# Optimization experiments

Hardware: AMD Instinct MI355X
Metric: run time of the kernel (lower is better)

The kernel has to match this reference:

```python
import jax, jax.numpy as jnp
import numpy as np

EPS = 1e-5
K = 20  # n. neighbors


def _lrelu(x):
    return jnp.where(x >= 0, x, 0.2 * x)


def _bn(x, gamma, beta):
    # training-mode batchnorm over all axes except channel axis 1
    axes = tuple(i for i in range(x.ndim) if i != 1)
    m = jnp.mean(x, axis=axes, keepdims=True)
    v = jnp.var(x, axis=axes, keepdims=True)
    shape = [1, x.shape[1]] + [1] * (x.ndim - 2)
    return (x - m) * jax.lax.rsqrt(v + EPS) * gamma.reshape(shape) + beta.reshape(shape)


def _knn(x, k):
    # x: (B, C, N) -> idx (B, N, k) of nearest neighbors (largest negative sq dist)
    xx = jnp.sum(x * x, axis=1)                      # (B, N)
    inner = jnp.einsum('bcn,bcm->bnm', x, x)          # (B, N, N)
    dist = -xx[:, :, None] + 2.0 * inner - xx[:, None, :]
    _, idx = jax.lax.top_k(dist, k)
    return idx


def _graph_feature(x, k):
    # x: (B, C, N) -> edge features (B, 2C, N, k)
    B = x.shape[0]
    idx = _knn(x, k)                                  # (B, N, k)
    xt = jnp.transpose(x, (0, 2, 1))                  # (B, N, C)
    nbr = xt[jnp.arange(B)[:, None, None], idx]       # (B, N, k, C)
    ctr = xt[:, :, None, :]                           # (B, N, 1, C)
    edge = jnp.concatenate([nbr - ctr, jnp.broadcast_to(ctr, nbr.shape)], axis=-1)
    return jnp.transpose(edge, (0, 3, 1, 2))          # (B, 2C, N, k)


def _conv1d(W, x):
    return jnp.einsum('oc,bcn->bon', W, x)


def _conv2d(W, x):
    return jnp.einsum('oc,bcnk->bonk', W, x)


def setup_inputs() -> dict:
    key = jax.random.key(0)
    ks = jax.random.split(key, 10)
    w = lambda k, s: jax.random.normal(k, s, jnp.float32) * 0.05
    d = {
        'x': jax.random.normal(ks[0], (4, 3, 4096), jnp.float32),
        'W1': w(ks[1], (64, 3)),
        'W2': w(ks[2], (64, 128)),
        'W3': w(ks[3], (64, 128)),
        'W4': w(ks[4], (512, 64)),
        'W5': w(ks[5], (512, 704)),
        'W6': w(ks[6], (256, 512)),
        'W7': w(ks[7], (128, 256)),
        'W8': w(ks[8], (2, 128)),
        'bias8': jnp.zeros((2,), jnp.float32),
    }
    bn_ch = [64, 64, 64, 512, 512, 256, 128]
    for i, c in enumerate(bn_ch, start=1):
        d[f'gamma{i}'] = jnp.ones((c,), jnp.float32)
        d[f'beta{i}'] = jnp.zeros((c,), jnp.float32)
    return d


def reference(x, W1, W2, W3, W4, W5, W6, W7, W8, bias8,
              gamma1, beta1, gamma2, beta2, gamma3, beta3, gamma4, beta4,
              gamma5, beta5, gamma6, beta6, gamma7, beta7):
    N = x.shape[2]
    x1 = _lrelu(_bn(_conv1d(W1, x), gamma1, beta1))                 # (B,64,N)
    e2 = _graph_feature(x1, K)                                      # (B,128,N,k)
    x2 = _lrelu(_bn(_conv2d(W2, e2), gamma2, beta2)).max(axis=-1)   # (B,64,N)
    e3 = _graph_feature(x2, K)
    x3 = _lrelu(_bn(_conv2d(W3, e3), gamma3, beta3)).max(axis=-1)   # (B,64,N)
    x6 = _lrelu(_bn(_conv1d(W4, x3), gamma4, beta4))                # (B,512,N)
    x6 = jnp.broadcast_to(x6.max(axis=-1, keepdims=True), (x6.shape[0], x6.shape[1], N))
    x7 = jnp.concatenate([x1, x2, x3, x6], axis=1)                  # (B,704,N)
    x7 = _lrelu(_bn(_conv1d(W5, x7), gamma5, beta5))
    x7 = _lrelu(_bn(_conv1d(W6, x7), gamma6, beta6))
    x7 = _lrelu(_bn(_conv1d(W7, x7), gamma7, beta7))
    return _conv1d(W8, x7) + bias8[None, :, None]                   # (B,2,N)
```

## Files before the change

### kernel.cpp

```cpp
#include <hip/hip_runtime.h>
#include <math.h>

#define NN 4096
#define BB 4
#define NPT (NN*BB)
#define KK 20
#define EPSB 1e-5f

#define AS_STRIDE 132
#define WS_STRIDE 68
#define SKEW(c) ((((((c)>>2)&7))<<2) + (((c)>>5)*28))

__device__ __forceinline__ float lrelu(float x){ return x >= 0.f ? x : 0.2f*x; }

__device__ __forceinline__ unsigned fkey(float x){
  unsigned u = __float_as_uint(x);
  return u ^ (unsigned)(((int)u >> 31) | 0x80000000);
}

__global__ void conv1_kernel(const float* __restrict__ x, const float* __restrict__ W1,
                             float* __restrict__ xcat){
  __shared__ float Wl[192];
  int tid = threadIdx.x;
  if (tid < 192) Wl[tid] = W1[tid];
  __syncthreads();
  int p = blockIdx.x*4 + (tid >> 6);
  int o = tid & 63;
  int b = p >> 12, n = p & 4095;
  const float* xb = x + (size_t)b*3*NN + n;
  float acc = Wl[o*3+0]*xb[0] + Wl[o*3+1]*xb[NN] + Wl[o*3+2]*xb[2*NN];
  xcat[(size_t)p*192 + o] = acc;
}

__global__ void stats_pm_kernel(const float* __restrict__ buf, int stride, int ofs,
                                float* __restrict__ psum, float* __restrict__ psumsq, int C){
  int tid = threadIdx.x;
  int lane = tid & 63, g = tid >> 6;
  int o = blockIdx.x*64 + lane;
  int p0 = blockIdx.y*256 + g*64;
  float s = 0.f, ss = 0.f;
  for (int i = 0; i < 64; ++i){
    float v = buf[(size_t)(p0+i)*stride + ofs + o];
    s += v; ss += v*v;
  }
  __shared__ float rs[4][64], rss[4][64];
  rs[g][lane] = s; rss[g][lane] = ss;
  __syncthreads();
  if (g == 0){
    s  = rs[0][lane]+rs[1][lane]+rs[2][lane]+rs[3][lane];
    ss = rss[0][lane]+rss[1][lane]+rss[2][lane]+rss[3][lane];
    psum[(size_t)blockIdx.y*C + o] = s;
    psumsq[(size_t)blockIdx.y*C + o] = ss;
  }
}

__global__ void bn_finalize_kernel(const float* __restrict__ psum, const float* __restrict__ psumsq,
                                   int nparts,
                                   const float* __restrict__ gamma, const float* __restrict__ beta,
                                   float* __restrict__ scale, float* __restrict__ shift,
                                   float invcnt, int C){
  int o = threadIdx.x + blockIdx.x*blockDim.x;
  if (o >= C) return;
  float s = 0.f, ss = 0.f;
  for (int i = 0; i < nparts; ++i){
    s  += psum[(size_t)i*C + o];
    ss += psumsq[(size_t)i*C + o];
  }
  float m = s*invcnt;
  float v = ss*invcnt - m*m;
  v = fmaxf(v, 0.f);
  float sc = gamma[o] * rsqrtf(v + EPSB);
  scale[o] = sc;
  shift[o] = beta[o] - m*sc;
}

__global__ void apply_bn_kernel(float* __restrict__ buf, int stride, int ofs, int log2C,
                                const float* __restrict__ scale, const float* __restrict__ shift){
  int i = blockIdx.x*256 + threadIdx.x;
  int o = i & ((1<<log2C)-1);
  int p = i >> log2C;
  size_t a = (size_t)p*stride + ofs + o;
  float e = buf[a]*scale[o] + shift[o];
  buf[a] = lrelu(e);
}

__global__ void xx_kernel(const float* __restrict__ xcat, int stride, int ofs,
                          float* __restrict__ xx){
  int p = blockIdx.x*256 + threadIdx.x;
  const float4* r = (const float4*)(xcat + (size_t)p*stride + ofs);
  float s = 0.f;
  #pragma unroll
  for (int i = 0; i < 16; ++i){ float4 v = r[i]; s += v.x*v.x + v.y*v.y + v.z*v.z + v.w*v.w; }
  xx[p] = s;
}

__global__ void __launch_bounds__(256, 2)
dist_kernel(const float* __restrict__ xcat, int ofs,
            const float* __restrict__ xx, float* __restrict__ dist,
            unsigned* __restrict__ gmaxp, int b){
  int bx = blockIdx.x, by = blockIdx.y;
  if (by > bx) return;
  __shared__ float As[64*AS_STRIDE + 64];
  __shared__ float Bs[64*AS_STRIDE + 64];
  int tid = threadIdx.x;
  int n0 = by*128, m0 = bx*128;
  const float* base = xcat + (size_t)b*NN*192 + ofs;
  int cgrp = (tid & 15)*4;
  float4 vin[8], vw[8];
  #pragma unroll
  for (int j = 0; j < 8; ++j){
    int row = (tid + 256*j) >> 4;
    vin[j] = *(const float4*)(base + (size_t)(n0+row)*192 + cgrp);
    vw[j]  = *(const float4*)(base + (size_t)(m0+row)*192 + cgrp);
  }
  #pragma unroll
  for (int j = 0; j < 8; ++j){
    int row = (tid + 256*j) >> 4, c4 = cgrp;
    float4 v = vin[j];
    As[(c4+0)*AS_STRIDE+SKEW(c4+0)+row]=v.x; As[(c4+1)*AS_STRIDE+SKEW(c4+1)+row]=v.y;
    As[(c4+2)*AS_STRIDE+SKEW(c4+2)+row]=v.z; As[(c4+3)*AS_STRIDE+SKEW(c4+3)+row]=v.w;
    float4 w = vw[j];
    Bs[(c4+0)*AS_STRIDE+SKEW(c4+0)+row]=w.x; Bs[(c4+1)*AS_STRIDE+SKEW(c4+1)+row]=w.y;
    Bs[(c4+2)*AS_STRIDE+SKEW(c4+2)+row]=w.z; Bs[(c4+3)*AS_STRIDE+SKEW(c4+3)+row]=w.w;
  }
  __syncthreads();
  int pA = (tid >> 4)*4, oB = (tid & 15)*4;
  float acc[8][8] = {};
  for (int c = 0; c < 64; ++c){
    const float* arow = &As[c*AS_STRIDE + SKEW(c)];
    const float* brow = &Bs[c*AS_STRIDE + SKEW(c)];
    float4 a0 = *(const float4*)&arow[pA];
    float4 a1 = *(const float4*)&arow[pA + 64];
    float4 b0 = *(const float4*)&brow[oB];
    float4 b1 = *(const float4*)&brow[oB + 64];
    float av[8] = {a0.x,a0.y,a0.z,a0.w,a1.x,a1.y,a1.z,a1.w};
    float bv[8] = {b0.x,b0.y,b0.z,b0.w,b1.x,b1.y,b1.z,b1.w};
    #pragma unroll
    for (int i = 0; i < 8; ++i)
      #pragma unroll
      for (int j = 0; j < 8; ++j)
        acc[i][j] += av[i]*bv[j];
  }
  float xmv[8], xnv[8];
  #pragma unroll
  for (int j = 0; j < 4; ++j){
    xmv[j]   = xx[b*NN + m0 + oB + j];
    xmv[4+j] = xx[b*NN + m0 + 64 + oB + j];
    xnv[j]   = xx[b*NN + n0 + pA + j];
    xnv[4+j] = xx[b*NN + n0 + 64 + pA + j];
  }
  #pragma unroll
  for (int h = 0; h < 2; ++h){
    #pragma unroll
    for (int i = 0; i < 4; ++i){
      int row = n0 + h*64 + pA + i;
      float xn = xnv[h*4 + i];
      int ai = h*4 + i;
      float4 w0, w1;
      w0.x = 2.f*acc[ai][0] - xn - xmv[0]; w0.y = 2.f*acc[ai][1] - xn - xmv[1];
      w0.z = 2.f*acc[ai][2] - xn - xmv[2]; w0.w = 2.f*acc[ai][3] - xn - xmv[3];
      w1.x = 2.f*acc[ai][4] - xn - xmv[4]; w1.y = 2.f*acc[ai][5] - xn - xmv[5];
      w1.z = 2.f*acc[ai][6] - xn - xmv[6]; w1.w = 2.f*acc[ai][7] - xn - xmv[7];
      float* drow = dist + (size_t)row*NN + m0;
      *(float4*)(drow + oB) = w0;
      *(float4*)(drow + 64 + oB) = w1;
      unsigned gm = fkey(w0.x), t;
      t = fkey(w0.y); if (t > gm) gm = t;
      t = fkey(w0.z); if (t > gm) gm = t;
      t = fkey(w0.w); if (t > gm) gm = t;
      t = fkey(w1.x); if (t > gm) gm = t;
      t = fkey(w1.y); if (t > gm) gm = t;
      t = fkey(w1.z); if (t > gm) gm = t;
      t = fkey(w1.w); if (t > gm) gm = t;
      gmaxp[(size_t)row*512 + (bx<<4) + (oB>>2)] = gm;
    }
  }
  if (bx != by){
    #pragma unroll
    for (int jh = 0; jh < 2; ++jh){
      #pragma unroll
      for (int jj = 0; jj < 4; ++jj){
        int j = jh*4 + jj;
        float xm = xmv[j];
        float4 lo, hi;
        lo.x = 2.f*acc[0][j] - xm - xnv[0];
        lo.y = 2.f*acc[1][j] - xm - xnv[1];
        lo.z = 2.f*acc[2][j] - xm - xnv[2];
        lo.w = 2.f*acc[3][j] - xm - xnv[3];
        hi.x = 2.f*acc[4][j] - xm - xnv[4];
        hi.y = 2.f*acc[5][j] - xm - xnv[5];
        hi.z = 2.f*acc[6][j] - xm - xnv[6];
        hi.w = 2.f*acc[7][j] - xm - xnv[7];
        int mrow = m0 + jh*64 + oB + jj;
        float* drow = dist + (size_t)mrow*NN + n0;
        *(float4*)(drow + pA) = lo;
        *(float4*)(drow + 64 + pA) = hi;
        unsigned gm = fkey(lo.x), t;
        t = fkey(lo.y); if (t > gm) gm = t;
        t = fkey(lo.z); if (t > gm) gm = t;
        t = fkey(lo.w); if (t > gm) gm = t;
        t = fkey(hi.x); if (t > gm) gm = t;
        t = fkey(hi.y); if (t > gm) gm = t;
        t = fkey(hi.z); if (t > gm) gm = t;
        t = fkey(hi.w); if (t > gm) gm = t;
        gmaxp[(size_t)mrow*512 + (by<<4) + (pA>>2)] = gm;
      }
    }
  }
}

__global__ void __launch_bounds__(256)
topk_kernel(const float* __restrict__ dist, const unsigned* __restrict__ gmax,
            int* __restrict__ idxout){
  __shared__ unsigned lv[4][256], li[4][256];
  __shared__ unsigned lcnt[4];
  int wv = threadIdx.x >> 6, lane = threadIdx.x & 63;
  int n = blockIdx.x*4 + wv;
  const unsigned* grow = gmax + (size_t)n*512;
  unsigned g[8];
  #pragma unroll
  for (int j = 0; j < 8; ++j) g[j] = grow[j*64 + lane];
  if (lane == 0) lcnt[wv] = 0u;
  unsigned prefix = 0u, act = 0xFFu; int need = KK; int tot = 512;
  for (int b = 31; b >= 16; --b){
    unsigned m = 0u;
    #pragma unroll
    for (int j = 0; j < 8; ++j) m |= ((g[j] >> b) & 1u) << j;
    unsigned c = (unsigned)__popc(m & act);
    #pragma unroll
    for (int s = 1; s < 64; s <<= 1) c += __shfl_xor(c, s);
    if ((int)c >= need){ act &= m; prefix |= (1u << b); tot = (int)c; }
    else { need -= (int)c; act &= ~m; tot -= (int)c; }
    if (KK - need + tot <= 44) break;
  }
  unsigned T = prefix;
  const float* drow = dist + (size_t)n*NN;
  #pragma unroll
  for (int j = 0; j < 8; ++j){
    if (g[j] >= T){
      int gid = j*64 + lane;
      int cbase = ((gid >> 4) << 7) + ((gid & 15) << 2);
      float4 v0 = *(const float4*)(drow + cbase);
      float4 v1 = *(const float4*)(drow + cbase + 64);
      unsigned k0=fkey(v0.x),k1=fkey(v0.y),k2=fkey(v0.z),k3=fkey(v0.w);
      unsigned k4=fkey(v1.x),k5=fkey(v1.y),k6=fkey(v1.z),k7=fkey(v1.w);
      int q = (k0>=T)+(k1>=T)+(k2>=T)+(k3>=T)+(k4>=T)+(k5>=T)+(k6>=T)+(k7>=T);
      unsigned pos = atomicAdd(&lcnt[wv], (unsigned)q);
      #define PUTC(kx,cofs) if (kx >= T){ if (pos < 256u){ lv[wv][pos]=kx; li[wv][pos]=(unsigned)(cbase+(cofs)); } pos++; }
      PUTC(k0,0) PUTC(k1,1) PUTC(k2,2) PUTC(k3,3)
      PUTC(k4,64) PUTC(k5,65) PUTC(k6,66) PUTC(k7,67)
      #undef PUTC
    }
  }
  unsigned C = lcnt[wv];
  int* orow = idxout + (size_t)n*KK;
  if (C <= 64u){
    unsigned kv = 0u, ki = 0xFFFFFFFFu;
    if (lane < (int)C){ kv = lv[wv][lane]; ki = li[wv][lane]; }
    #pragma unroll
    for (int k = 2; k <= 64; k <<= 1){
      #pragma unroll
      for (int j2 = k >> 1; j2 > 0; j2 >>= 1){
        unsigned ov = __shfl_xor(kv, j2);
        unsigned oi = __shfl_xor(ki, j2);
        bool iLower = ((lane & j2) == 0);
        bool dirDesc = ((lane & k) == 0);
        bool mineGr = (kv > ov) || (kv == ov && ki < oi);
        bool keep = dirDesc ? (iLower ? mineGr : !mineGr)
                            : (iLower ? !mineGr : mineGr);
        kv = keep ? kv : ov;
        ki = keep ? ki : oi;
      }
    }
    if (lane < KK) orow[lane] = (int)ki;
  } else {
    unsigned rv[KK], ri[KK];
    #pragma unroll
    for (int q = 0; q < KK; ++q){ rv[q]=0u; ri[q]=0xFFFFFFFFu; }
    #pragma unroll
    for (int j = 0; j < 8; ++j){
      if (g[j] >= T){
        int gid = j*64 + lane;
        int cbase = ((gid >> 4) << 7) + ((gid & 15) << 2);
        float4 v0 = *(const float4*)(drow + cbase);
        float4 v1 = *(const float4*)(drow + cbase + 64);
        float f0[8] = {v0.x,v0.y,v0.z,v0.w,v1.x,v1.y,v1.z,v1.w};
        #pragma unroll
        for (int t = 0; t < 8; ++t){
          unsigned u = fkey(f0[t]);
          unsigned ix = (unsigned)(cbase + ((t < 4) ? t : (60 + t)));
          bool beat = (u > rv[KK-1]) || (u == rv[KK-1] && ix < ri[KK-1]);
          if (u >= T && beat){
            unsigned pv = u, pi = ix;
            #pragma unroll
            for (int p = 0; p < KK; ++p){
              bool keep2 = (rv[p] > pv) || (rv[p] == pv && ri[p] < pi);
              unsigned nv = keep2 ? rv[p] : pv;
              unsigned ni = keep2 ? ri[p] : pi;
              pv = keep2 ? pv : rv[p];
              pi = keep2 ? pi : ri[p];
              rv[p] = nv; ri[p] = ni;
            }
          }
        }
      }
    }
    for (int q = 0; q < KK; ++q){
      unsigned bv = rv[0], bi = ri[0];
      #pragma unroll
      for (int s = 1; s < 64; s <<= 1){
        unsigned ov = __shfl_xor(bv, s);
        unsigned oi = __shfl_xor(bi, s);
        bool take = (ov > bv) || (ov == bv && oi < bi);
        bv = take ? ov : bv;
        bi = take ? oi : bi;
      }
      if (rv[0] == bv && ri[0] == bi){
        #pragma unroll
        for (int p = 0; p < KK-1; ++p){ rv[p] = rv[p+1]; ri[p] = ri[p+1]; }
        rv[KK-1] = 0u; ri[KK-1] = 0xFFFFFFFFu;
      }
      if (lane == 0) orow[q] = (int)bi;
    }
  }
}

__global__ void ut_kernel(const float* __restrict__ xcat, int ofs, const float* __restrict__ W,
                          float* __restrict__ U, float* __restrict__ T){
  __shared__ float Wl[64*129];
  int tid = threadIdx.x;
  for (int i = tid; i < 64*128; i += 256){
    int o = i >> 7, c = i & 127;
    Wl[o*129 + c] = W[i];
  }
  __syncthreads();
  int g = tid >> 6, lane = tid & 63;
  int p = blockIdx.x*4 + g;
  float xv = xcat[(size_t)p*192 + ofs + lane];
  const float* wr = Wl + lane*129;
  float u = 0.f, t = 0.f;
  for (int c = 0; c < 64; ++c){
    float xc = __shfl(xv, c);
    float wa = wr[c], wb = wr[64+c];
    u += wa*xc;
    t += (wb - wa)*xc;
  }
  U[(size_t)p*64 + lane] = u;
  T[(size_t)p*64 + lane] = t;
}

__global__ void gather_kernel(const float* __restrict__ U, const float* __restrict__ T,
                              const int* __restrict__ idx,
                              float* __restrict__ psum, float* __restrict__ psumsq,
                              float* __restrict__ vmax, float* __restrict__ vmin){
  int tid = threadIdx.x;
  int g = tid >> 6, lane = tid & 63;
  int p0 = blockIdx.x*64 + g*16;
  float s = 0.f, ss = 0.f;
  for (int pi = 0; pi < 16; ++pi){
    int p = p0 + pi;
    int base = (p >> 12) << 12;
    float t = T[(size_t)p*64 + lane];
    const int* ir = idx + (size_t)p*KK;
    float mx = -INFINITY, mn = INFINITY;
    for (int k = 0; k < KK; ++k){
      int j = ir[k];
      float v = U[(size_t)(base + j)*64 + lane] + t;
      s += v; ss += v*v;
      mx = fmaxf(mx, v); mn = fminf(mn, v);
    }
    vmax[(size_t)p*64 + lane] = mx;
    vmin[(size_t)p*64 + lane] = mn;
  }
  __shared__ float rs[4][64], rss[4][64];
  rs[g][lane] = s; rss[g][lane] = ss;
  __syncthreads();
  if (g == 0){
    s  = rs[0][lane]+rs[1][lane]+rs[2][lane]+rs[3][lane];
    ss = rss[0][lane]+rss[1][lane]+rss[2][lane]+rss[3][lane];
    psum[(size_t)blockIdx.x*64 + lane] = s;
    psumsq[(size_t)blockIdx.x*64 + lane] = ss;
  }
}

__global__ void gapply_kernel(const float* __restrict__ vmax, const float* __restrict__ vmin,
                              const float* __restrict__ scale, const float* __restrict__ shift,
                              float* __restrict__ xcat, int ofs){
  int i = blockIdx.x*256 + threadIdx.x;
  int p = i >> 6, o = i & 63;
  float s = scale[o];
  float v = (s >= 0.f) ? vmax[i] : vmin[i];
  xcat[(size_t)p*192 + ofs + o] = lrelu(s*v + shift[o]);
}

__global__ void __launch_bounds__(256, 2)
mm_kernel(const float* __restrict__ in, int inStride, int inOfs,
          const float* __restrict__ W, int wStride,
          float* __restrict__ out, int outStride,
          const float* __restrict__ bias, int O, int I,
          const float* __restrict__ bnScale, const float* __restrict__ bnShift){
  __shared__ float As[64*AS_STRIDE + 64];
  __shared__ float Ws[64*WS_STRIDE + 64];
  int tid = threadIdx.x;
  int p0 = blockIdx.x*128, o0 = blockIdx.y*64;
  int psub = (tid >> 4)*8, osub = (tid & 15)*4;
  int cgrp = (tid & 15)*4;
  float acc[8][4] = {};
  for (int cc = 0; cc < I; cc += 64){
    float4 sc4 = make_float4(1.f,1.f,1.f,1.f), sh4 = make_float4(0.f,0.f,0.f,0.f);
    if (bnScale){
      sc4 = *(const float4*)(bnScale + cc + cgrp);
      sh4 = *(const float4*)(bnShift + cc + cgrp);
    }
    float4 vin[8], vw[4];
    #pragma unroll
    for (int j = 0; j < 8; ++j){
      int row = (tid + 256*j) >> 4;
      vin[j] = *(const float4*)(in + (size_t)(p0+row)*inStride + inOfs + cc + cgrp);
    }
    #pragma unroll
    for (int j = 0; j < 4; ++j){
      int row = (tid + 256*j) >> 4;
      vw[j] = *(const float4*)(W + (size_t)(o0+row)*wStride + cc + cgrp);
    }
    #pragma unroll
    for (int j = 0; j < 8; ++j){
      int row = (tid + 256*j) >> 4, c4 = cgrp;
      float4 v = vin[j];
      if (bnScale){
        v.x = lrelu(v.x*sc4.x + sh4.x); v.y = lrelu(v.y*sc4.y + sh4.y);
        v.z = lrelu(v.z*sc4.z + sh4.z); v.w = lrelu(v.w*sc4.w + sh4.w);
      }
      As[(c4+0)*AS_STRIDE+SKEW(c4+0)+row]=v.x; As[(c4+1)*AS_STRIDE+SKEW(c4+1)+row]=v.y;
      As[(c4+2)*AS_STRIDE+SKEW(c4+2)+row]=v.z; As[(c4+3)*AS_STRIDE+SKEW(c4+3)+row]=v.w;
    }
    #pragma unroll
    for (int j = 0; j < 4; ++j){
      int row = (tid + 256*j) >> 4, c4 = cgrp;
      float4 v = vw[j];
      Ws[(c4+0)*WS_STRIDE+SKEW(c4+0)+row]=v.x; Ws[(c4+1)*WS_STRIDE+SKEW(c4+1)+row]=v.y;
      Ws[(c4+2)*WS_STRIDE+SKEW(c4+2)+row]=v.z; Ws[(c4+3)*WS_STRIDE+SKEW(c4+3)+row]=v.w;
    }
    __syncthreads();
    for (int c = 0; c < 64; ++c){
      const float* arow = &As[c*AS_STRIDE + SKEW(c)];
      const float* brow = &Ws[c*WS_STRIDE + SKEW(c)];
      float4 a0 = *(const float4*)&arow[psub];
      float4 a1 = *(const float4*)&arow[psub + 4];
      float4 bb = *(const float4*)&brow[osub];
      float av[8] = {a0.x,a0.y,a0.z,a0.w,a1.x,a1.y,a1.z,a1.w};
      float bv[4] = {bb.x,bb.y,bb.z,bb.w};
      #pragma unroll
      for (int i = 0; i < 8; ++i)
        #pragma unroll
        for (int j = 0; j < 4; ++j)
          acc[i][j] += av[i]*bv[j];
    }
    __syncthreads();
  }
  int bIdx = p0 >> 12;
  float bb0=0.f, bb1=0.f, bb2=0.f, bb3=0.f;
  if (bias){
    bb0 = bias[bIdx*O + o0 + osub + 0];
    bb1 = bias[bIdx*O + o0 + osub + 1];
    bb2 = bias[bIdx*O + o0 + osub + 2];
    bb3 = bias[bIdx*O + o0 + osub + 3];
  }
  #pragma unroll
  for (int i = 0; i < 8; ++i){
    float4 w;
    w.x = acc[i][0]+bb0; w.y = acc[i][1]+bb1; w.z = acc[i][2]+bb2; w.w = acc[i][3]+bb3;
    *(float4*)(out + (size_t)(p0+psub+i)*outStride + o0 + osub) = w;
  }
}

__global__ void __launch_bounds__(256, 2)
mm128_kernel(const float* __restrict__ in, int inStride, int inOfs,
             const float* __restrict__ W, int wStride,
             float* __restrict__ out, int outStride,
             const float* __restrict__ bias, int O, int I,
             const float* __restrict__ bnScale, const float* __restrict__ bnShift){
  __shared__ float As[64*AS_STRIDE + 64];
  __shared__ float Ws[64*AS_STRIDE + 64];
  int tid = threadIdx.x;
  int p0 = blockIdx.x*128, o0 = blockIdx.y*128;
  int pA = (tid >> 4)*4, oB = (tid & 15)*4;
  int cgrp = (tid & 15)*4;
  float acc[8][8] = {};
  for (int cc = 0; cc < I; cc += 64){
    float4 sc4 = make_float4(1.f,1.f,1.f,1.f), sh4 = make_float4(0.f,0.f,0.f,0.f);
    if (bnScale){
      sc4 = *(const float4*)(bnScale + cc + cgrp);
      sh4 = *(const float4*)(bnShift + cc + cgrp);
    }
    float4 vin[8], vw[8];
    #pragma unroll
    for (int j = 0; j < 8; ++j){
      int row = (tid + 256*j) >> 4;
      vin[j] = *(const float4*)(in + (size_t)(p0+row)*inStride + inOfs + cc + cgrp);
      vw[j]  = *(const float4*)(W + (size_t)(o0+row)*wStride + cc + cgrp);
    }
    #pragma unroll
    for (int j = 0; j < 8; ++j){
      int row = (tid + 256*j) >> 4, c4 = cgrp;
      float4 v = vin[j];
      if (bnScale){
        v.x = lrelu(v.x*sc4.x + sh4.x); v.y = lrelu(v.y*sc4.y + sh4.y);
        v.z = lrelu(v.z*sc4.z + sh4.z); v.w = lrelu(v.w*sc4.w + sh4.w);
      }
      As[(c4+0)*AS_STRIDE+SKEW(c4+0)+row]=v.x; As[(c4+1)*AS_STRIDE+SKEW(c4+1)+row]=v.y;
      As[(c4+2)*AS_STRIDE+SKEW(c4+2)+row]=v.z; As[(c4+3)*AS_STRIDE+SKEW(c4+3)+row]=v.w;
      float4 w = vw[j];
      Ws[(c4+0)*AS_STRIDE+SKEW(c4+0)+row]=w.x; Ws[(c4+1)*AS_STRIDE+SKEW(c4+1)+row]=w.y;
      Ws[(c4+2)*AS_STRIDE+SKEW(c4+2)+row]=w.z; Ws[(c4+3)*AS_STRIDE+SKEW(c4+3)+row]=w.w;
    }
    __syncthreads();
    for (int c = 0; c < 64; ++c){
      const float* arow = &As[c*AS_STRIDE + SKEW(c)];
      const float* brow = &Ws[c*AS_STRIDE + SKEW(c)];
      float4 a0 = *(const float4*)&arow[pA];
      float4 a1 = *(const float4*)&arow[pA + 64];
      float4 b0 = *(const float4*)&brow[oB];
      float4 b1 = *(const float4*)&brow[oB + 64];
      float av[8] = {a0.x,a0.y,a0.z,a0.w,a1.x,a1.y,a1.z,a1.w};
      float bv[8] = {b0.x,b0.y,b0.z,b0.w,b1.x,b1.y,b1.z,b1.w};
      #pragma unroll
      for (int i = 0; i < 8; ++i)
        #pragma unroll
        for (int j = 0; j < 8; ++j)
          acc[i][j] += av[i]*bv[j];
    }
    __syncthreads();
  }
  int bIdx = p0 >> 12;
  float bb[8] = {0.f,0.f,0.f,0.f,0.f,0.f,0.f,0.f};
  if (bias){
    #pragma unroll
    for (int j = 0; j < 4; ++j){
      bb[j]   = bias[bIdx*O + o0 + oB + j];
      bb[4+j] = bias[bIdx*O + o0 + 64 + oB + j];
    }
  }
  #pragma unroll
  for (int h = 0; h < 2; ++h){
    #pragma unroll
    for (int i = 0; i < 4; ++i){
      int row = p0 + h*64 + pA + i;
      int ai = h*4 + i;
      float4 w0, w1;
      w0.x = acc[ai][0]+bb[0]; w0.y = acc[ai][1]+bb[1];
      w0.z = acc[ai][2]+bb[2]; w0.w = acc[ai][3]+bb[3];
      w1.x = acc[ai][4]+bb[4]; w1.y = acc[ai][5]+bb[5];
      w1.z = acc[ai][6]+bb[6]; w1.w = acc[ai][7]+bb[7];
      float* orow = out + (size_t)row*outStride + o0;
      *(float4*)(orow + oB) = w0;
      *(float4*)(orow + 64 + oB) = w1;
    }
  }
}

__global__ void __launch_bounds__(256, 2)
conv4stats_kernel(const float* __restrict__ xcat, const float* __restrict__ W4,
                  float* __restrict__ psum, float* __restrict__ psumsq,
                  float* __restrict__ pmax, float* __restrict__ pmin){
  __shared__ float As[64*AS_STRIDE + 64];
  __shared__ float Ws[64*AS_STRIDE + 64];
  int tid = threadIdx.x;
  int p0 = blockIdx.x*128, o0 = blockIdx.y*128;
  int pA = (tid >> 4)*4, oB = (tid & 15)*4;
  int cgrp = (tid & 15)*4;
  float4 vin[8], vw[8];
  #pragma unroll
  for (int j = 0; j < 8; ++j){
    int row = (tid + 256*j) >> 4;
    vin[j] = *(const float4*)(xcat + (size_t)(p0+row)*192 + 128 + cgrp);
    vw[j]  = *(const float4*)(W4 + (size_t)(o0+row)*64 + cgrp);
  }
  #pragma unroll
  for (int j = 0; j < 8; ++j){
    int row = (tid + 256*j) >> 4, c4 = cgrp;
    float4 v = vin[j];
    As[(c4+0)*AS_STRIDE+SKEW(c4+0)+row]=v.x; As[(c4+1)*AS_STRIDE+SKEW(c4+1)+row]=v.y;
    As[(c4+2)*AS_STRIDE+SKEW(c4+2)+row]=v.z; As[(c4+3)*AS_STRIDE+SKEW(c4+3)+row]=v.w;
    float4 w = vw[j];
    Ws[(c4+0)*AS_STRIDE+SKEW(c4+0)+row]=w.x; Ws[(c4+1)*AS_STRIDE+SKEW(c4+1)+row]=w.y;
    Ws[(c4+2)*AS_STRIDE+SKEW(c4+2)+row]=w.z; Ws[(c4+3)*AS_STRIDE+SKEW(c4+3)+row]=w.w;
  }
  __syncthreads();
  float acc[8][8] = {};
  for (int c = 0; c < 64; ++c){
    const float* arow = &As[c*AS_STRIDE + SKEW(c)];
    const float* brow = &Ws[c*AS_STRIDE + SKEW(c)];
    float4 a0 = *(const float4*)&arow[pA];
    float4 a1 = *(const float4*)&arow[pA + 64];
    float4 b0 = *(const float4*)&brow[oB];
    float4 b1 = *(const float4*)&brow[oB + 64];
    float av[8] = {a0.x,a0.y,a0.z,a0.w,a1.x,a1.y,a1.z,a1.w};
    float bv[8] = {b0.x,b0.y,b0.z,b0.w,b1.x,b1.y,b1.z,b1.w};
    #pragma unroll
    for (int i = 0; i < 8; ++i)
      #pragma unroll
      for (int j = 0; j < 8; ++j)
        acc[i][j] += av[i]*bv[j];
  }
  float cs[8], cq[8], cmx[8], cmn[8];
  #pragma unroll
  for (int j = 0; j < 8; ++j){
    float s = 0.f, q = 0.f, mx = -INFINITY, mn = INFINITY;
    #pragma unroll
    for (int i = 0; i < 8; ++i){
      float v = acc[i][j];
      s += v; q += v*v; mx = fmaxf(mx, v); mn = fminf(mn, v);
    }
    cs[j]=s; cq[j]=q; cmx[j]=mx; cmn[j]=mn;
  }
  __syncthreads();
  int r = tid >> 4;
  #pragma unroll
  for (int j = 0; j < 8; ++j){
    int col = (j < 4) ? (oB + j) : (64 + oB + (j-4));
    As[r*128 + col]        = cs[j];
    As[2048 + r*128 + col] = cq[j];
    Ws[r*128 + col]        = cmx[j];
    Ws[2048 + r*128 + col] = cmn[j];
  }
  __syncthreads();
  if (tid < 128){
    float ts = 0.f, tq = 0.f, tm = -INFINITY, tn = INFINITY;
    for (int rr = 0; rr < 16; ++rr){
      ts += As[rr*128 + tid];
      tq += As[2048 + rr*128 + tid];
      tm = fmaxf(tm, Ws[rr*128 + tid]);
      tn = fminf(tn, Ws[2048 + rr*128 + tid]);
    }
    size_t slot = (size_t)blockIdx.x*512 + o0 + tid;
    psum[slot] = ts; psumsq[slot] = tq; pmax[slot] = tm; pmin[slot] = tn;
  }
}

__global__ void x6v_kernel(const float* __restrict__ pmax, const float* __restrict__ pmin,
                           const float* __restrict__ scale, const float* __restrict__ shift,
                           float* __restrict__ x6v){
  int t = blockIdx.x*256 + threadIdx.x;
  int b = t >> 9, o = t & 511;
  float mx = -INFINITY, mn = INFINITY;
  for (int pt = b*32; pt < b*32+32; ++pt){
    mx = fmaxf(mx, pmax[(size_t)pt*512 + o]);
    mn = fminf(mn, pmin[(size_t)pt*512 + o]);
  }
  float s = scale[o];
  float v = (s >= 0.f) ? mx : mn;
  x6v[t] = lrelu(s*v + shift[o]);
}

__global__ void bias5_kernel(const float* __restrict__ W5, const float* __restrict__ x6v,
                             float* __restrict__ b5){
  __shared__ float xl[512];
  int tid = threadIdx.x;
  int t = blockIdx.x*256 + tid;
  int b = t >> 9, o = t & 511;
  for (int i = tid; i < 512; i += 256) xl[i] = x6v[(b<<9) + i];
  __syncthreads();
  const float* wr = W5 + (size_t)o*704 + 192;
  float acc = 0.f;
  for (int c = 0; c < 512; ++c) acc += wr[c]*xl[c];
  b5[t] = acc;
}

__global__ void conv8_kernel(const float* __restrict__ r7, const float* __restrict__ W8,
                             const float* __restrict__ bias8,
                             const float* __restrict__ scale, const float* __restrict__ shift,
                             float* __restrict__ out){
  __shared__ float Wl[256];
  __shared__ float scl[128], shl[128];
  int tid = threadIdx.x;
  Wl[tid] = W8[tid];
  if (tid < 128){ scl[tid] = scale[tid]; shl[tid] = shift[tid]; }
  __syncthreads();
  int p = blockIdx.x*256 + tid;
  int b = p >> 12, n = p & 4095;
  const float4* row = (const float4*)(r7 + (size_t)p*128);
  float a0 = 0.f, a1 = 0.f;
  #pragma unroll
  for (int i = 0; i < 32; ++i){
    float4 v = row[i];
    v.x = lrelu(v.x*scl[i*4+0] + shl[i*4+0]);
    v.y = lrelu(v.y*scl[i*4+1] + shl[i*4+1]);
    v.z = lrelu(v.z*scl[i*4+2] + shl[i*4+2]);
    v.w = lrelu(v.w*scl[i*4+3] + shl[i*4+3]);
    a0 += v.x*Wl[i*4] + v.y*Wl[i*4+1] + v.z*Wl[i*4+2] + v.w*Wl[i*4+3];
    a1 += v.x*Wl[128+i*4] + v.y*Wl[128+i*4+1] + v.z*Wl[128+i*4+2] + v.w*Wl[128+i*4+3];
  }
  out[(size_t)(b*2+0)*NN + n] = a0 + bias8[0];
  out[(size_t)(b*2+1)*NN + n] = a1 + bias8[1];
}

extern "C" void kernel_launch(void* const* d_in, const int* in_sizes, int n_in,
                              void* d_out, int out_size, void* d_ws, size_t ws_size,
                              hipStream_t stream){
  const float* x     = (const float*)d_in[0];
  const float* W1    = (const float*)d_in[1];
  const float* W2    = (const float*)d_in[2];
  const float* W3    = (const float*)d_in[3];
  const float* W4    = (const float*)d_in[4];
  const float* W5    = (const float*)d_in[5];
  const float* W6    = (const float*)d_in[6];
  const float* W7    = (const float*)d_in[7];
  const float* W8    = (const float*)d_in[8];
  const float* bias8 = (const float*)d_in[9];
  const float* gamma[8]; const float* beta[8];
  for (int i = 1; i <= 7; ++i){
    gamma[i] = (const float*)d_in[10 + 2*(i-1)];
    beta[i]  = (const float*)d_in[11 + 2*(i-1)];
  }
  float* out = (float*)d_out;

  float* ws = (float*)d_ws;
  size_t off = 0;
  float* xcat  = ws + off; off += (size_t)NPT*192;
  float* U     = ws + off; off += (size_t)NPT*64;
  float* T     = ws + off; off += (size_t)NPT*64;
  float* xx    = ws + off; off += NPT;
  int*   idx   = (int*)(ws + off); off += (size_t)NPT*KK;
  float* psum  = ws + off; off += 128*512;
  float* psumsq= ws + off; off += 128*512;
  float* pmax  = ws + off; off += 128*512;
  float* pmin  = ws + off; off += 128*512;
  float* scale = ws + off; off += 512;
  float* shift = ws + off; off += 512;
  float* x6v   = ws + off; off += 2048;
  float* b5    = ws + off; off += 2048;
  float* big   = ws + off;
  float* dist  = big;
  float* vmaxB = big;
  float* vminB = big + (size_t)NPT*64;
  float* r5    = big;
  float* r6    = big + (size_t)NPT*512;
  float* r7    = big + (size_t)NPT*512 + (size_t)NPT*256;
  unsigned* gmaxU = (unsigned*)U;

  conv1_kernel<<<NPT/4, 256, 0, stream>>>(x, W1, xcat);
  stats_pm_kernel<<<dim3(1,64), 256, 0, stream>>>(xcat, 192, 0, psum, psumsq, 64);
  bn_finalize_kernel<<<1, 64, 0, stream>>>(psum, psumsq, 64, gamma[1], beta[1], scale, shift, 1.f/16384.f, 64);
  apply_bn_kernel<<<NPT*64/256, 256, 0, stream>>>(xcat, 192, 0, 6, scale, shift);

  xx_kernel<<<NPT/256, 256, 0, stream>>>(xcat, 192, 0, xx);
  for (int b = 0; b < BB; ++b){
    dist_kernel<<<dim3(32,32), 256, 0, stream>>>(xcat, 0, xx, dist, gmaxU, b);
    topk_kernel<<<NN/4, 256, 0, stream>>>(dist, gmaxU, idx + (size_t)b*NN*KK);
  }

  ut_kernel<<<NPT/4, 256, 0, stream>>>(xcat, 0, W2, U, T);
  gather_kernel<<<256, 256, 0, stream>>>(U, T, idx, psum, psumsq, vmaxB, vminB);
  bn_finalize_kernel<<<1, 64, 0, stream>>>(psum, psumsq, 256, gamma[2], beta[2], scale, shift, 1.f/327680.f, 64);
  gapply_kernel<<<NPT*64/256, 256, 0, stream>>>(vmaxB, vminB, scale, shift, xcat, 64);

  xx_kernel<<<NPT/256, 256, 0, stream>>>(xcat, 192, 64, xx);
  for (int b = 0; b < BB; ++b){
    dist_kernel<<<dim3(32,32), 256, 0, stream>>>(xcat, 64, xx, dist, gmaxU, b);
    topk_kernel<<<NN/4, 256, 0, stream>>>(dist, gmaxU, idx + (size_t)b*NN*KK);
  }

  ut_kernel<<<NPT/4, 256, 0, stream>>>(xcat, 64, W3, U, T);
  gather_kernel<<<256, 256, 0, stream>>>(U, T, idx, psum, psumsq, vmaxB, vminB);
  bn_finalize_kernel<<<1, 64, 0, stream>>>(psum, psumsq, 256, gamma[3], beta[3], scale, shift, 1.f/327680.f, 64);
  gapply_kernel<<<NPT*64/256, 256, 0, stream>>>(vmaxB, vminB, scale, shift, xcat, 128);

  conv4stats_kernel<<<dim3(NPT/128, 4), 256, 0, stream>>>(xcat, W4, psum, psumsq, pmax, pmin);
  bn_finalize_kernel<<<1, 512, 0, stream>>>(psum, psumsq, 128, gamma[4], beta[4], scale, shift, 1.f/16384.f, 512);
  x6v_kernel<<<8, 256, 0, stream>>>(pmax, pmin, scale, shift, x6v);
  bias5_kernel<<<8, 256, 0, stream>>>(W5, x6v, b5);

  mm128_kernel<<<dim3(NPT/128, 4), 256, 0, stream>>>(xcat, 192, 0, W5, 704, r5, 512, b5, 512, 192, nullptr, nullptr);
  stats_pm_kernel<<<dim3(8,64), 256, 0, stream>>>(r5, 512, 0, psum, psumsq, 512);
  bn_finalize_kernel<<<1, 512, 0, stream>>>(psum, psumsq, 64, gamma[5], beta[5], scale, shift, 1.f/16384.f, 512);

  mm_kernel<<<dim3(NPT/128, 4), 256, 0, stream>>>(r5, 512, 0, W6, 512, r6, 256, nullptr, 256, 512, scale, shift);
  stats_pm_kernel<<<dim3(4,64), 256, 0, stream>>>(r6, 256, 0, psum, psumsq, 256);
  bn_finalize_kernel<<<1, 256, 0, stream>>>(psum, psumsq, 64, gamma[6], beta[6], scale, shift, 1.f/16384.f, 256);

  mm_kernel<<<dim3(NPT/128, 2), 256, 0, stream>>>(r6, 256, 0, W7, 256, r7, 128, nullptr, 128, 256, scale, shift);
  stats_pm_kernel<<<dim3(2,64), 256, 0, stream>>>(r7, 128, 0, psum, psumsq, 128);
  bn_finalize_kernel<<<1, 128, 0, stream>>>(psum, psumsq, 64, gamma[7], beta[7], scale, shift, 1.f/16384.f, 128);

  conv8_kernel<<<NPT/256, 256, 0, stream>>>(r7, W8, bias8, scale, shift, out);
}
```

Measured before the change: 1.097 ms.

## Drop materialized distance matrix; recompute candidate distances in top-k from features

The distance kernel no longer writes the full N×N distance matrix. It only emits per-8-column group maxima, and all batches run in one launch through a z grid dimension. The top-k kernel recomputes exact dot-product distances for the surviving candidate groups straight from the 64-channel features, which removes the large distance-matrix write and read. The cost is extra arithmetic and scattered feature reads for each candidate. Small differences in float rounding against the GEMM path could shift ties between the group maximum and the recomputed values.

```diff
diff --git a/kernel.cpp b/kernel.cpp
--- a/kernel.cpp
+++ b/kernel.cpp
@@ -95,10 +95,9 @@
 }
 
 __global__ void __launch_bounds__(256, 2)
-dist_kernel(const float* __restrict__ xcat, int ofs,
-            const float* __restrict__ xx, float* __restrict__ dist,
-            unsigned* __restrict__ gmaxp, int b){
-  int bx = blockIdx.x, by = blockIdx.y;
+gmax_kernel(const float* __restrict__ xcat, int ofs,
+            const float* __restrict__ xx, unsigned* __restrict__ gmaxp){
+  int bx = blockIdx.x, by = blockIdx.y, b = blockIdx.z;
   if (by > bx) return;
   __shared__ float As[64*AS_STRIDE + 64];
   __shared__ float Bs[64*AS_STRIDE + 64];
@@ -161,9 +160,6 @@
       w0.z = 2.f*acc[ai][2] - xn - xmv[2]; w0.w = 2.f*acc[ai][3] - xn - xmv[3];
       w1.x = 2.f*acc[ai][4] - xn - xmv[4]; w1.y = 2.f*acc[ai][5] - xn - xmv[5];
       w1.z = 2.f*acc[ai][6] - xn - xmv[6]; w1.w = 2.f*acc[ai][7] - xn - xmv[7];
-      float* drow = dist + (size_t)row*NN + m0;
-      *(float4*)(drow + oB) = w0;
-      *(float4*)(drow + 64 + oB) = w1;
       unsigned gm = fkey(w0.x), t;
       t = fkey(w0.y); if (t > gm) gm = t;
       t = fkey(w0.z); if (t > gm) gm = t;
@@ -172,7 +168,7 @@
       t = fkey(w1.y); if (t > gm) gm = t;
       t = fkey(w1.z); if (t > gm) gm = t;
       t = fkey(w1.w); if (t > gm) gm = t;
-      gmaxp[(size_t)row*512 + (bx<<4) + (oB>>2)] = gm;
+      gmaxp[(size_t)(b*NN + row)*512 + (bx<<4) + (oB>>2)] = gm;
     }
   }
   if (bx != by){
@@ -192,9 +188,6 @@
         hi.z = 2.f*acc[6][j] - xm - xnv[6];
         hi.w = 2.f*acc[7][j] - xm - xnv[7];
         int mrow = m0 + jh*64 + oB + jj;
-        float* drow = dist + (size_t)mrow*NN + n0;
-        *(float4*)(drow + pA) = lo;
-        *(float4*)(drow + 64 + pA) = hi;
         unsigned gm = fkey(lo.x), t;
         t = fkey(lo.y); if (t > gm) gm = t;
         t = fkey(lo.z); if (t > gm) gm = t;
@@ -203,57 +196,86 @@
         t = fkey(hi.y); if (t > gm) gm = t;
         t = fkey(hi.z); if (t > gm) gm = t;
         t = fkey(hi.w); if (t > gm) gm = t;
-        gmaxp[(size_t)mrow*512 + (by<<4) + (pA>>2)] = gm;
+        gmaxp[(size_t)(b*NN + mrow)*512 + (by<<4) + (pA>>2)] = gm;
       }
     }
   }
 }
 
 __global__ void __launch_bounds__(256)
-topk_kernel(const float* __restrict__ dist, const unsigned* __restrict__ gmax,
-            int* __restrict__ idxout){
+topk_kernel(const float* __restrict__ xcat, int ofs, const float* __restrict__ xx,
+            const unsigned* __restrict__ gmax, int* __restrict__ idxout){
   __shared__ unsigned lv[4][256], li[4][256];
   __shared__ unsigned lcnt[4];
+  __shared__ float xnl[4][64];
   int wv = threadIdx.x >> 6, lane = threadIdx.x & 63;
+  int b = blockIdx.z;
   int n = blockIdx.x*4 + wv;
-  const unsigned* grow = gmax + (size_t)n*512;
+  const float* base = xcat + (size_t)b*NN*192 + ofs;
+  const unsigned* grow = gmax + (size_t)(b*NN + n)*512;
   unsigned g[8];
   #pragma unroll
   for (int j = 0; j < 8; ++j) g[j] = grow[j*64 + lane];
+  xnl[wv][lane] = base[(size_t)n*192 + lane];
+  float xxn = xx[b*NN + n];
   if (lane == 0) lcnt[wv] = 0u;
   unsigned prefix = 0u, act = 0xFFu; int need = KK; int tot = 512;
-  for (int b = 31; b >= 16; --b){
+  for (int bit = 31; bit >= 16; --bit){
     unsigned m = 0u;
     #pragma unroll
-    for (int j = 0; j < 8; ++j) m |= ((g[j] >> b) & 1u) << j;
+    for (int j = 0; j < 8; ++j) m |= ((g[j] >> bit) & 1u) << j;
     unsigned c = (unsigned)__popc(m & act);
     #pragma unroll
     for (int s = 1; s < 64; s <<= 1) c += __shfl_xor(c, s);
-    if ((int)c >= need){ act &= m; prefix |= (1u << b); tot = (int)c; }
+    if ((int)c >= need){ act &= m; prefix |= (1u << bit); tot = (int)c; }
     else { need -= (int)c; act &= ~m; tot -= (int)c; }
     if (KK - need + tot <= 44) break;
   }
   unsigned T = prefix;
-  const float* drow = dist + (size_t)n*NN;
+  const float* xrow = xnl[wv];
   #pragma unroll
   for (int j = 0; j < 8; ++j){
     if (g[j] >= T){
       int gid = j*64 + lane;
       int cbase = ((gid >> 4) << 7) + ((gid & 15) << 2);
-      float4 v0 = *(const float4*)(drow + cbase);
-      float4 v1 = *(const float4*)(drow + cbase + 64);
-      unsigned k0=fkey(v0.x),k1=fkey(v0.y),k2=fkey(v0.z),k3=fkey(v0.w);
-      unsigned k4=fkey(v1.x),k5=fkey(v1.y),k6=fkey(v1.z),k7=fkey(v1.w);
-      int q = (k0>=T)+(k1>=T)+(k2>=T)+(k3>=T)+(k4>=T)+(k5>=T)+(k6>=T)+(k7>=T);
+      int mcol[8];
+      const float* xmp[8];
+      float dacc[8] = {0.f,0.f,0.f,0.f,0.f,0.f,0.f,0.f};
+      #pragma unroll
+      for (int t = 0; t < 8; ++t){
+        mcol[t] = cbase + ((t < 4) ? t : (60 + t));
+        xmp[t] = base + (size_t)mcol[t]*192;
+      }
+      for (int c = 0; c < 64; c += 4){
+        float4 a4 = *(const float4*)(xrow + c);
+        #pragma unroll
+        for (int t = 0; t < 8; ++t){
+          float4 b4 = *(const float4*)(xmp[t] + c);
+          dacc[t] += a4.x*b4.x; dacc[t] += a4.y*b4.y;
+          dacc[t] += a4.z*b4.z; dacc[t] += a4.w*b4.w;
+        }
+      }
+      unsigned keys[8];
+      #pragma unroll
+      for (int t = 0; t < 8; ++t){
+        float dd = 2.f*dacc[t] - xxn - xx[b*NN + mcol[t]];
+        keys[t] = fkey(dd);
+      }
+      int q = 0;
+      #pragma unroll
+      for (int t = 0; t < 8; ++t) q += (keys[t] >= T);
       unsigned pos = atomicAdd(&lcnt[wv], (unsigned)q);
-      #define PUTC(kx,cofs) if (kx >= T){ if (pos < 256u){ lv[wv][pos]=kx; li[wv][pos]=(unsigned)(cbase+(cofs)); } pos++; }
-      PUTC(k0,0) PUTC(k1,1) PUTC(k2,2) PUTC(k3,3)
-      PUTC(k4,64) PUTC(k5,65) PUTC(k6,66) PUTC(k7,67)
-      #undef PUTC
+      #pragma unroll
+      for (int t = 0; t < 8; ++t){
+        if (keys[t] >= T){
+          if (pos < 256u){ lv[wv][pos] = keys[t]; li[wv][pos] = (unsigned)mcol[t]; }
+          pos++;
+        }
+      }
     }
   }
   unsigned C = lcnt[wv];
-  int* orow = idxout + (size_t)n*KK;
+  int* orow = idxout + (size_t)(b*NN + n)*KK;
   if (C <= 64u){
     unsigned kv = 0u, ki = 0xFFFFFFFFu;
     if (lane < (int)C){ kv = lv[wv][lane]; ki = li[wv][lane]; }
@@ -282,13 +304,20 @@
       if (g[j] >= T){
         int gid = j*64 + lane;
         int cbase = ((gid >> 4) << 7) + ((gid & 15) << 2);
-        float4 v0 = *(const float4*)(drow + cbase);
-        float4 v1 = *(const float4*)(drow + cbase + 64);
-        float f0[8] = {v0.x,v0.y,v0.z,v0.w,v1.x,v1.y,v1.z,v1.w};
         #pragma unroll
         for (int t = 0; t < 8; ++t){
-          unsigned u = fkey(f0[t]);
-          unsigned ix = (unsigned)(cbase + ((t < 4) ? t : (60 + t)));
+          int m = cbase + ((t < 4) ? t : (60 + t));
+          const float* xm = base + (size_t)m*192;
+          float dacc = 0.f;
+          for (int c = 0; c < 64; c += 4){
+            float4 a4 = *(const float4*)(xrow + c);
+            float4 b4 = *(const float4*)(xm + c);
+            dacc += a4.x*b4.x; dacc += a4.y*b4.y;
+            dacc += a4.z*b4.z; dacc += a4.w*b4.w;
+          }
+          float dd = 2.f*dacc - xxn - xx[b*NN + m];
+          unsigned u = fkey(dd);
+          unsigned ix = (unsigned)m;
           bool beat = (u > rv[KK-1]) || (u == rv[KK-1] && ix < ri[KK-1]);
           if (u >= T && beat){
             unsigned pv = u, pi = ix;
@@ -731,13 +760,12 @@
   float* x6v   = ws + off; off += 2048;
   float* b5    = ws + off; off += 2048;
   float* big   = ws + off;
-  float* dist  = big;
+  unsigned* gmaxB = (unsigned*)big;
   float* vmaxB = big;
   float* vminB = big + (size_t)NPT*64;
   float* r5    = big;
   float* r6    = big + (size_t)NPT*512;
   float* r7    = big + (size_t)NPT*512 + (size_t)NPT*256;
-  unsigned* gmaxU = (unsigned*)U;
 
   conv1_kernel<<<NPT/4, 256, 0, stream>>>(x, W1, xcat);
   stats_pm_kernel<<<dim3(1,64), 256, 0, stream>>>(xcat, 192, 0, psum, psumsq, 64);
@@ -745,10 +773,8 @@
   apply_bn_kernel<<<NPT*64/256, 256, 0, stream>>>(xcat, 192, 0, 6, scale, shift);
 
   xx_kernel<<<NPT/256, 256, 0, stream>>>(xcat, 192, 0, xx);
-  for (int b = 0; b < BB; ++b){
-    dist_kernel<<<dim3(32,32), 256, 0, stream>>>(xcat, 0, xx, dist, gmaxU, b);
-    topk_kernel<<<NN/4, 256, 0, stream>>>(dist, gmaxU, idx + (size_t)b*NN*KK);
-  }
+  gmax_kernel<<<dim3(32,32,BB), 256, 0, stream>>>(xcat, 0, xx, gmaxB);
+  topk_kernel<<<dim3(NN/4,1,BB), 256, 0, stream>>>(xcat, 0, xx, gmaxB, idx);
 
   ut_kernel<<<NPT/4, 256, 0, stream>>>(xcat, 0, W2, U, T);
   gather_kernel<<<256, 256, 0, stream>>>(U, T, idx, psum, psumsq, vmaxB, vminB);
@@ -756,10 +782,8 @@
   gapply_kernel<<<NPT*64/256, 256, 0, stream>>>(vmaxB, vminB, scale, shift, xcat, 64);
 
   xx_kernel<<<NPT/256, 256, 0, stream>>>(xcat, 192, 64, xx);
-  for (int b = 0; b < BB; ++b){
-    dist_kernel<<<dim3(32,32), 256, 0, stream>>>(xcat, 64, xx, dist, gmaxU, b);
-    topk_kernel<<<NN/4, 256, 0, stream>>>(dist, gmaxU, idx + (size_t)b*NN*KK);
-  }
+  gmax_kernel<<<dim3(32,32,BB), 256, 0, stream>>>(xcat, 64, xx, gmaxB);
+  topk_kernel<<<dim3(NN/4,1,BB), 256, 0, stream>>>(xcat, 64, xx, gmaxB, idx);
 
   ut_kernel<<<NPT/4, 256, 0, stream>>>(xcat, 64, W3, U, T);
   gather_kernel<<<256, 256, 0, stream>>>(U, T, idx, psum, psumsq, vmaxB, vminB);
```

Result: slower. 1.867 ms (+70.3%).

## Shrink GEMM tiles and K-chunks to raise block count for the pointwise convs

Applied to the files above, without the earlier changes.

Changes the channel chunk in the generic GEMM kernel from 64 to 32. It also moves the trailing barrier so the next chunk's global loads are issued before the sync. The 128x128 mm128 kernel is replaced with the 128x64 mm_kernel for conv5, and a new 64x64-tile mm64 kernel handles conv6 and conv7. The aim is more blocks and less shared memory per block, for better occupancy and latency hiding on these small GEMMs. The cost is lower register reuse per thread and more barriers per unit of work.

```diff
diff --git a/kernel.cpp b/kernel.cpp
--- a/kernel.cpp
+++ b/kernel.cpp
@@ -399,33 +399,34 @@
           float* __restrict__ out, int outStride,
           const float* __restrict__ bias, int O, int I,
           const float* __restrict__ bnScale, const float* __restrict__ bnShift){
-  __shared__ float As[64*AS_STRIDE + 64];
-  __shared__ float Ws[64*WS_STRIDE + 64];
+  __shared__ float As[32*AS_STRIDE + 64];
+  __shared__ float Ws[32*WS_STRIDE + 64];
   int tid = threadIdx.x;
   int p0 = blockIdx.x*128, o0 = blockIdx.y*64;
   int psub = (tid >> 4)*8, osub = (tid & 15)*4;
-  int cgrp = (tid & 15)*4;
+  int cgrp = (tid & 7)*4;
   float acc[8][4] = {};
-  for (int cc = 0; cc < I; cc += 64){
+  for (int cc = 0; cc < I; cc += 32){
     float4 sc4 = make_float4(1.f,1.f,1.f,1.f), sh4 = make_float4(0.f,0.f,0.f,0.f);
     if (bnScale){
       sc4 = *(const float4*)(bnScale + cc + cgrp);
       sh4 = *(const float4*)(bnShift + cc + cgrp);
     }
-    float4 vin[8], vw[4];
-    #pragma unroll
-    for (int j = 0; j < 8; ++j){
-      int row = (tid + 256*j) >> 4;
+    float4 vin[4], vw[2];
+    #pragma unroll
+    for (int j = 0; j < 4; ++j){
+      int row = (tid + 256*j) >> 3;
       vin[j] = *(const float4*)(in + (size_t)(p0+row)*inStride + inOfs + cc + cgrp);
     }
     #pragma unroll
+    for (int j = 0; j < 2; ++j){
+      int row = (tid + 256*j) >> 3;
+      vw[j] = *(const float4*)(W + (size_t)(o0+row)*wStride + cc + cgrp);
+    }
+    if (cc) __syncthreads();
+    #pragma unroll
     for (int j = 0; j < 4; ++j){
-      int row = (tid + 256*j) >> 4;
-      vw[j] = *(const float4*)(W + (size_t)(o0+row)*wStride + cc + cgrp);
-    }
-    #pragma unroll
-    for (int j = 0; j < 8; ++j){
-      int row = (tid + 256*j) >> 4, c4 = cgrp;
+      int row = (tid + 256*j) >> 3, c4 = cgrp;
       float4 v = vin[j];
       if (bnScale){
         v.x = lrelu(v.x*sc4.x + sh4.x); v.y = lrelu(v.y*sc4.y + sh4.y);
@@ -435,14 +436,14 @@
       As[(c4+2)*AS_STRIDE+SKEW(c4+2)+row]=v.z; As[(c4+3)*AS_STRIDE+SKEW(c4+3)+row]=v.w;
     }
     #pragma unroll
-    for (int j = 0; j < 4; ++j){
-      int row = (tid + 256*j) >> 4, c4 = cgrp;
+    for (int j = 0; j < 2; ++j){
+      int row = (tid + 256*j) >> 3, c4 = cgrp;
       float4 v = vw[j];
       Ws[(c4+0)*WS_STRIDE+SKEW(c4+0)+row]=v.x; Ws[(c4+1)*WS_STRIDE+SKEW(c4+1)+row]=v.y;
       Ws[(c4+2)*WS_STRIDE+SKEW(c4+2)+row]=v.z; Ws[(c4+3)*WS_STRIDE+SKEW(c4+3)+row]=v.w;
     }
     __syncthreads();
-    for (int c = 0; c < 64; ++c){
+    for (int c = 0; c < 32; ++c){
       const float* arow = &As[c*AS_STRIDE + SKEW(c)];
       const float* brow = &Ws[c*WS_STRIDE + SKEW(c)];
       float4 a0 = *(const float4*)&arow[psub];
@@ -456,7 +457,6 @@
         for (int j = 0; j < 4; ++j)
           acc[i][j] += av[i]*bv[j];
     }
-    __syncthreads();
   }
   int bIdx = p0 >> 12;
   float bb0=0.f, bb1=0.f, bb2=0.f, bb3=0.f;
@@ -475,87 +475,66 @@
 }
 
 __global__ void __launch_bounds__(256, 2)
-mm128_kernel(const float* __restrict__ in, int inStride, int inOfs,
-             const float* __restrict__ W, int wStride,
-             float* __restrict__ out, int outStride,
-             const float* __restrict__ bias, int O, int I,
-             const float* __restrict__ bnScale, const float* __restrict__ bnShift){
-  __shared__ float As[64*AS_STRIDE + 64];
-  __shared__ float Ws[64*AS_STRIDE + 64];
-  int tid = threadIdx.x;
-  int p0 = blockIdx.x*128, o0 = blockIdx.y*128;
-  int pA = (tid >> 4)*4, oB = (tid & 15)*4;
-  int cgrp = (tid & 15)*4;
-  float acc[8][8] = {};
-  for (int cc = 0; cc < I; cc += 64){
+mm64_kernel(const float* __restrict__ in, int inStride, int inOfs,
+            const float* __restrict__ W, int wStride,
+            float* __restrict__ out, int outStride,
+            int O, int I,
+            const float* __restrict__ bnScale, const float* __restrict__ bnShift){
+  __shared__ float As[32*WS_STRIDE + 64];
+  __shared__ float Ws[32*WS_STRIDE + 64];
+  int tid = threadIdx.x;
+  int p0 = blockIdx.x*64, o0 = blockIdx.y*64;
+  int psub = (tid >> 4)*4, osub = (tid & 15)*4;
+  int cgrp = (tid & 7)*4;
+  float acc[4][4] = {};
+  for (int cc = 0; cc < I; cc += 32){
     float4 sc4 = make_float4(1.f,1.f,1.f,1.f), sh4 = make_float4(0.f,0.f,0.f,0.f);
     if (bnScale){
       sc4 = *(const float4*)(bnScale + cc + cgrp);
       sh4 = *(const float4*)(bnShift + cc + cgrp);
     }
-    float4 vin[8], vw[8];
-    #pragma unroll
-    for (int j = 0; j < 8; ++j){
-      int row = (tid + 256*j) >> 4;
+    float4 vin[2], vw[2];
+    #pragma unroll
+    for (int j = 0; j < 2; ++j){
+      int row = (tid + 256*j) >> 3;
       vin[j] = *(const float4*)(in + (size_t)(p0+row)*inStride + inOfs + cc + cgrp);
       vw[j]  = *(const float4*)(W + (size_t)(o0+row)*wStride + cc + cgrp);
     }
-    #pragma unroll
-    for (int j = 0; j < 8; ++j){
-      int row = (tid + 256*j) >> 4, c4 = cgrp;
+    if (cc) __syncthreads();
+    #pragma unroll
+    for (int j = 0; j < 2; ++j){
+      int row = (tid + 256*j) >> 3, c4 = cgrp;
       float4 v = vin[j];
       if (bnScale){
         v.x = lrelu(v.x*sc4.x + sh4.x); v.y = lrelu(v.y*sc4.y + sh4.y);
         v.z = lrelu(v.z*sc4.z + sh4.z); v.w = lrelu(v.w*sc4.w + sh4.w);
       }
-      As[(c4+0)*AS_STRIDE+SKEW(c4+0)+row]=v.x; As[(c4+1)*AS_STRIDE+SKEW(c4+1)+row]=v.y;
-      As[(c4+2)*AS_STRIDE+SKEW(c4+2)+row]=v.z; As[(c4+3)*AS_STRIDE+SKEW(c4+3)+row]=v.w;
+      As[(c4+0)*WS_STRIDE+SKEW(c4+0)+row]=v.x; As[(c4+1)*WS_STRIDE+SKEW(c4+1)+row]=v.y;
+      As[(c4+2)*WS_STRIDE+SKEW(c4+2)+row]=v.z; As[(c4+3)*WS_STRIDE+SKEW(c4+3)+row]=v.w;
       float4 w = vw[j];
-      Ws[(c4+0)*AS_STRIDE+SKEW(c4+0)+row]=w.x; Ws[(c4+1)*AS_STRIDE+SKEW(c4+1)+row]=w.y;
-      Ws[(c4+2)*AS_STRIDE+SKEW(c4+2)+row]=w.z; Ws[(c4+3)*AS_STRIDE+SKEW(c4+3)+row]=w.w;
+      Ws[(c4+0)*WS_STRIDE+SKEW(c4+0)+row]=w.x; Ws[(c4+1)*WS_STRIDE+SKEW(c4+1)+row]=w.y;
+      Ws[(c4+2)*WS_STRIDE+SKEW(c4+2)+row]=w.z; Ws[(c4+3)*WS_STRIDE+SKEW(c4+3)+row]=w.w;
     }
     __syncthreads();
-    for (int c = 0; c < 64; ++c){
-      const float* arow = &As[c*AS_STRIDE + SKEW(c)];
-      const float* brow = &Ws[c*AS_STRIDE + SKEW(c)];
-      float4 a0 = *(const float4*)&arow[pA];
-      float4 a1 = *(const float4*)&arow[pA + 64];
-      float4 b0 = *(const float4*)&brow[oB];
-      float4 b1 = *(const float4*)&brow[oB + 64];
-      float av[8] = {a0.x,a0.y,a0.z,a0.w,a1.x,a1.y,a1.z,a1.w};
-      float bv[8] = {b0.x,b0.y,b0.z,b0.w,b1.x,b1.y,b1.z,b1.w};
+    for (int c = 0; c < 32; ++c){
+      const float* arow = &As[c*WS_STRIDE + SKEW(c)];
+      const float* brow = &Ws[c*WS_STRIDE + SKEW(c)];
+      float4 a0 = *(const float4*)&arow[psub];
+      float4 bb = *(const float4*)&brow[osub];
+      float av[4] = {a0.x,a0.y,a0.z,a0.w};
+      float bv[4] = {bb.x,bb.y,bb.z,bb.w};
       #pragma unroll
-      for (int i = 0; i < 8; ++i)
+      for (int i = 0; i < 4; ++i)
         #pragma unroll
-        for (int j = 0; j < 8; ++j)
+        for (int j = 0; j < 4; ++j)
           acc[i][j] += av[i]*bv[j];
     }
-    __syncthreads();
-  }
-  int bIdx = p0 >> 12;
-  float bb[8] = {0.f,0.f,0.f,0.f,0.f,0.f,0.f,0.f};
-  if (bias){
-    #pragma unroll
-    for (int j = 0; j < 4; ++j){
-      bb[j]   = bias[bIdx*O + o0 + oB + j];
-      bb[4+j] = bias[bIdx*O + o0 + 64 + oB + j];
-    }
-  }
-  #pragma unroll
-  for (int h = 0; h < 2; ++h){
-    #pragma unroll
-    for (int i = 0; i < 4; ++i){
-      int row = p0 + h*64 + pA + i;
-      int ai = h*4 + i;
-      float4 w0, w1;
-      w0.x = acc[ai][0]+bb[0]; w0.y = acc[ai][1]+bb[1];
-      w0.z = acc[ai][2]+bb[2]; w0.w = acc[ai][3]+bb[3];
-      w1.x = acc[ai][4]+bb[4]; w1.y = acc[ai][5]+bb[5];
-      w1.z = acc[ai][6]+bb[6]; w1.w = acc[ai][7]+bb[7];
-      float* orow = out + (size_t)row*outStride + o0;
-      *(float4*)(orow + oB) = w0;
-      *(float4*)(orow + 64 + oB) = w1;
-    }
+  }
+  #pragma unroll
+  for (int i = 0; i < 4; ++i){
+    float4 w;
+    w.x = acc[i][0]; w.y = acc[i][1]; w.z = acc[i][2]; w.w = acc[i][3];
+    *(float4*)(out + (size_t)(p0+psub+i)*outStride + o0 + osub) = w;
   }
 }
 
@@ -771,15 +750,15 @@
   x6v_kernel<<<8, 256, 0, stream>>>(pmax, pmin, scale, shift, x6v);
   bias5_kernel<<<8, 256, 0, stream>>>(W5, x6v, b5);
 
-  mm128_kernel<<<dim3(NPT/128, 4), 256, 0, stream>>>(xcat, 192, 0, W5, 704, r5, 512, b5, 512, 192, nullptr, nullptr);
+  mm_kernel<<<dim3(NPT/128, 8), 256, 0, stream>>>(xcat, 192, 0, W5, 704, r5, 512, b5, 512, 192, nullptr, nullptr);
   stats_pm_kernel<<<dim3(8,64), 256, 0, stream>>>(r5, 512, 0, psum, psumsq, 512);
   bn_finalize_kernel<<<1, 512, 0, stream>>>(psum, psumsq, 64, gamma[5], beta[5], scale, shift, 1.f/16384.f, 512);
 
-  mm_kernel<<<dim3(NPT/128, 4), 256, 0, stream>>>(r5, 512, 0, W6, 512, r6, 256, nullptr, 256, 512, scale, shift);
+  mm64_kernel<<<dim3(NPT/64, 4), 256, 0, stream>>>(r5, 512, 0, W6, 512, r6, 256, 256, 512, scale, shift);
   stats_pm_kernel<<<dim3(4,64), 256, 0, stream>>>(r6, 256, 0, psum, psumsq, 256);
   bn_finalize_kernel<<<1, 256, 0, stream>>>(psum, psumsq, 64, gamma[6], beta[6], scale, shift, 1.f/16384.f, 256);
 
-  mm_kernel<<<dim3(NPT/128, 2), 256, 0, stream>>>(r6, 256, 0, W7, 256, r7, 128, nullptr, 128, 256, scale, shift);
+  mm64_kernel<<<dim3(NPT/64, 2), 256, 0, stream>>>(r6, 256, 0, W7, 256, r7, 128, 128, 256, scale, shift);
   stats_pm_kernel<<<dim3(2,64), 256, 0, stream>>>(r7, 128, 0, psum, psumsq, 128);
   bn_finalize_kernel<<<1, 128, 0, stream>>>(psum, psumsq, 64, gamma[7], beta[7], scale, shift, 1.f/16384.f, 128);
 
```

Result: no change. 1.089 ms (-0.7%).
